# Optimization experiments

Measured on AMD Instinct MI355X. Metric: run time of the kernel, lower is better.

Reference implementation:

```python
import jax, jax.numpy as jnp
import numpy as np

BITS = 4
GROUP_SIZE = 128
INF, OUTF, TOKENS = 4096, 11008, 256


def setup_inputs() -> dict:
    key = jax.random.key(0)
    k1, k2, k3, k4, k5 = jax.random.split(key, 5)
    n_groups = INF // GROUP_SIZE  # 32
    x = jax.random.normal(k1, (TOKENS, INF), dtype=jnp.float32)
    qweight = jax.random.randint(k2, (INF // 32 * BITS, OUTF), 0, 2**31 - 1, dtype=jnp.int32)
    qzeros = jax.random.randint(k3, (n_groups, OUTF // 32 * BITS), 0, 2**31 - 1, dtype=jnp.int32)
    scales = jax.random.uniform(k4, (n_groups, OUTF), dtype=jnp.float32, minval=1e-3, maxval=2e-2)
    bias = jax.random.normal(k5, (OUTF,), dtype=jnp.float32)
    return {"x": x, "qweight": qweight, "qzeros": qzeros, "scales": scales, "bias": bias}


def _dequantize(qweight, qzeros, scales):
    """Unpack int4 nibbles and build the fp32 weight [infeatures, outfeatures]."""
    shifts = jnp.arange(0, 32, BITS, dtype=jnp.int32)  # [8]
    mask = (1 << BITS) - 1
    out_f = qweight.shape[1]
    # qweight row packs 8 consecutive in-features -> [K, O] int in [0, 15]
    w = ((qweight[:, None, :] >> shifts[None, :, None]) & mask).reshape(-1, out_f)
    # qzeros col packs 8 consecutive out-features; stored as (zero - 1)
    n_groups = qzeros.shape[0]
    z = (((qzeros[:, :, None] >> shifts[None, None, :]) & mask) + 1).reshape(n_groups, out_f)
    g_idx = jnp.arange(w.shape[0], dtype=jnp.int32) // GROUP_SIZE  # [K]
    return (w - z[g_idx]).astype(jnp.float32) * scales[g_idx]


def reference(x, qweight, qzeros, scales, bias):
    W = _dequantize(qweight, qzeros, scales)  # [infeatures, outfeatures]
    return x @ W + bias  # [tokens, outfeatures]
```

## Files before the change

### kernel.cpp

```cpp
#include <hip/hip_runtime.h>
#include <stdint.h>

#define TOKENS  256
#define INF     4096
#define OUTF    11008
#define NGROUPS 32
#define NPHASE  16
#define NTH     256

typedef __attribute__((ext_vector_type(2))) _Float16 f16x2;
typedef __attribute__((ext_vector_type(8))) _Float16 f16x8;
typedef __attribute__((ext_vector_type(2))) __fp16   pkh2;
typedef __attribute__((ext_vector_type(4))) float    f32x4;

union U32H2 { uint32_t u; f16x2 h; };
union H8    { f16x2 h2[4]; f16x8 h8; };
union PK    { pkh2 p; f16x2 h; };

__device__ __forceinline__ void gl2lds16(const void* g, void* l) {
    __builtin_amdgcn_global_load_lds(
        (const __attribute__((address_space(1))) uint32_t*)g,
        (__attribute__((address_space(3))) uint32_t*)l, 16, 0, 0);
}

__device__ __forceinline__ int Fswz(int m4) {
    return (m4 & 0xF) | (((m4 ^ (m4 >> 1)) & 1) << 4);
}

__global__ __launch_bounds__(NTH)
void cvt_x(const float* __restrict__ x, _Float16* __restrict__ x16) {
    const int t   = blockIdx.x * NTH + threadIdx.x;
    const int row = t >> 9;
    const int c   = t & 511;
    const float* p = x + (size_t)row * INF + c * 8;
    f32x4 v0 = *(const f32x4*)p;
    f32x4 v1 = *(const f32x4*)(p + 4);
    H8 o; PK k0, k1, k2, k3;
    k0.p = __builtin_amdgcn_cvt_pkrtz(v0[0], v1[0]);
    k1.p = __builtin_amdgcn_cvt_pkrtz(v0[1], v1[1]);
    k2.p = __builtin_amdgcn_cvt_pkrtz(v0[2], v1[2]);
    k3.p = __builtin_amdgcn_cvt_pkrtz(v0[3], v1[3]);
    o.h2[0] = k0.h; o.h2[1] = k1.h; o.h2[2] = k2.h; o.h2[3] = k3.h;
    *(f16x8*)(x16 + (size_t)row * INF + c * 8) = o.h8;
}

__global__ __launch_bounds__(NTH, 2)
void qlin_main(const _Float16* __restrict__ x16,
               const uint32_t* __restrict__ qweight,
               const uint32_t* __restrict__ qzeros,
               const float* __restrict__ scales,
               const float* __restrict__ bias,
               float* __restrict__ out)
{
    __shared__ alignas(16) _Float16 As[2][64 * 256];

    const int tid = threadIdx.x;
    const int bx  = blockIdx.x >> 2;
    const int by  = blockIdx.x & 3;

    const int lane = tid & 63;
    const int quad = lane >> 4;
    const int l16  = lane & 15;
    const int wv   = tid >> 6;

    const int rowoff = (tid >> 5) & 7;
    const int sclin  = tid & 31;
    const int row0   = by * 64;
    const uint32_t aoffE = (uint32_t)((row0 + rowoff)     * (INF * 2) + (sclin ^ Fswz(rowoff))     * 16);
    const uint32_t aoffO = (uint32_t)((row0 + 8 + rowoff) * (INF * 2) + (sclin ^ Fswz(8 + rowoff)) * 16);
    const char* x16b = (const char*)x16;
    _Float16* ldsW = &As[0][0];
    const int ldsSlotBase = wv * 512;

    const int col0 = bx * 128 + wv * 32 + l16;
    const int col1 = col0 + 16;
    const int bOff0 = quad * OUTF + col0;
    const int bOff1 = quad * OUTF + col1;
    const int zsh = (col0 & 7) * 4;

    const int fsw = Fswz(l16);

    f32x4 acc[4][2];
#pragma unroll
    for (int mi = 0; mi < 4; ++mi)
#pragma unroll
        for (int nf = 0; nf < 2; ++nf)
            acc[mi][nf] = f32x4{0.f, 0.f, 0.f, 0.f};

    uint32_t Breg[2][16];
    float    sS[2][4];
    uint32_t qZ[2][4];

#pragma unroll
    for (int ii = 0; ii < 4; ++ii) {
        gl2lds16(x16b + aoffE + ii * 131072, ldsW + (2 * ii)     * 2048 + ldsSlotBase);
        gl2lds16(x16b + aoffO + ii * 131072, ldsW + (2 * ii + 1) * 2048 + ldsSlotBase);
    }
#pragma unroll
    for (int s = 0; s < 8; ++s) {
        const uint32_t* qp = qweight + (size_t)(s * 4) * OUTF;
        Breg[0][2 * s + 0] = qp[bOff0];
        Breg[0][2 * s + 1] = qp[bOff1];
    }
    sS[0][0] = scales[0 * OUTF + col0]; sS[0][1] = scales[0 * OUTF + col1];
    sS[0][2] = scales[1 * OUTF + col0]; sS[0][3] = scales[1 * OUTF + col1];
    qZ[0][0] = qzeros[0 * (OUTF / 8) + (col0 >> 3)]; qZ[0][1] = qzeros[0 * (OUTF / 8) + (col1 >> 3)];
    qZ[0][2] = qzeros[1 * (OUTF / 8) + (col0 >> 3)]; qZ[0][3] = qzeros[1 * (OUTF / 8) + (col1 >> 3)];
    __syncthreads();

#pragma unroll
    for (int p = 0; p < NPHASE; ++p) {
        const int par = p & 1;
        const int np  = par ^ 1;

        if (p < NPHASE - 1) {
            const int pn = p + 1;
            const uint32_t pb = (uint32_t)(pn * 512);
            _Float16* ldsN = ldsW + np * 16384;
#pragma unroll
            for (int ii = 0; ii < 4; ++ii) {
                gl2lds16(x16b + aoffE + ii * 131072 + pb, ldsN + (2 * ii)     * 2048 + ldsSlotBase);
                gl2lds16(x16b + aoffO + ii * 131072 + pb, ldsN + (2 * ii + 1) * 2048 + ldsSlotBase);
            }
            const uint32_t* qpb = qweight + (size_t)(pn * 32) * OUTF;
#pragma unroll
            for (int s = 0; s < 8; ++s) {
                const uint32_t* qp = qpb + (size_t)(s * 4) * OUTF;
                Breg[np][2 * s + 0] = qp[bOff0];
                Breg[np][2 * s + 1] = qp[bOff1];
            }
            const int g0 = 2 * pn, g1 = 2 * pn + 1;
            sS[np][0] = scales[g0 * OUTF + col0]; sS[np][1] = scales[g0 * OUTF + col1];
            sS[np][2] = scales[g1 * OUTF + col0]; sS[np][3] = scales[g1 * OUTF + col1];
            qZ[np][0] = qzeros[g0 * (OUTF / 8) + (col0 >> 3)]; qZ[np][1] = qzeros[g0 * (OUTF / 8) + (col1 >> 3)];
            qZ[np][2] = qzeros[g1 * (OUTF / 8) + (col0 >> 3)]; qZ[np][3] = qzeros[g1 * (OUTF / 8) + (col1 >> 3)];
        }

        f16x2 hs2[2][2], hz2[2][2];
#pragma unroll
        for (int gh = 0; gh < 2; ++gh)
#pragma unroll
            for (int nf = 0; nf < 2; ++nf) {
                const float s = sS[par][gh * 2 + nf];
                const int   z = (int)((qZ[par][gh * 2 + nf] >> zsh) & 15u) + 1025;
                const _Float16 hs = (_Float16)s;
                const _Float16 hz = (_Float16)(-(float)z);
                hs2[gh][nf] = f16x2{hs, hs};
                hz2[gh][nf] = f16x2{hz, hz};
            }

        const _Float16* buf = ldsW + par * 16384;
#pragma unroll
        for (int s = 0; s < 8; ++s) {
            const int gh = s >> 2;
            f16x8 af[4];
#pragma unroll
            for (int mi = 0; mi < 4; ++mi) {
                const int m  = mi * 16 + l16;
                const int sc = (s * 4 + quad) ^ fsw;
                af[mi] = *(const f16x8*)(buf + m * 256 + sc * 8);
            }
#pragma unroll
            for (int nf = 0; nf < 2; ++nf) {
                const uint32_t q = Breg[par][2 * s + nf];
                H8 b;
#pragma unroll
                for (int j = 0; j < 4; ++j) {
                    U32H2 u;
                    u.u = ((q >> (4 * j)) & 0x000F000Fu) | 0x64006400u;
                    b.h2[j] = (u.h + hz2[gh][nf]) * hs2[gh][nf];
                }
#pragma unroll
                for (int mi = 0; mi < 4; ++mi)
                    acc[mi][nf] = __builtin_amdgcn_mfma_f32_16x16x32_f16(
                        af[mi], b.h8, acc[mi][nf], 0, 0, 0);
            }
        }

        __syncthreads();
    }

#pragma unroll
    for (int nf = 0; nf < 2; ++nf) {
        const int col = (nf == 0) ? col0 : col1;
        const float bv = bias[col];
#pragma unroll
        for (int mi = 0; mi < 4; ++mi) {
            const int r0 = by * 64 + mi * 16 + quad * 4;
#pragma unroll
            for (int rg = 0; rg < 4; ++rg)
                out[(size_t)(r0 + rg) * OUTF + col] = acc[mi][nf][rg] + bv;
        }
    }
}

__global__ __launch_bounds__(NTH, 2)
void qlin_fb(const float* __restrict__ x,
             const uint32_t* __restrict__ qweight,
             const uint32_t* __restrict__ qzeros,
             const float* __restrict__ scales,
             const float* __restrict__ bias,
             float* __restrict__ out)
{
    __shared__ alignas(16) _Float16 Asb[64][40];
    __shared__ alignas(16) _Float16 Bsb[128][40];
    const int tid = threadIdx.x;
    const int bx = blockIdx.x, by = blockIdx.y;
    const int am = tid >> 2, ar = tid & 3;
    const float* xrow = x + (size_t)(by * 64 + am) * INF + ar * 8;
    const int bc = tid & 127, br = tid >> 7;
    const int bn = bx * 128 + bc;
    const int bswz = (bc >> 3) & 3;
    const int lane = tid & 63, quad = lane >> 4, l16 = lane & 15;
    const int wv = tid >> 6, wm = wv >> 1, wn = wv & 1;
    f32x4 acc[2][4];
#pragma unroll
    for (int i = 0; i < 2; ++i)
#pragma unroll
        for (int j = 0; j < 4; ++j) acc[i][j] = f32x4{0.f, 0.f, 0.f, 0.f};
    f32x4 pa0 = *(const f32x4*)(xrow + 0);
    f32x4 pa1 = *(const f32x4*)(xrow + 4);
    uint32_t pq0 = qweight[(size_t)br * OUTF + bn];
    uint32_t pq1 = qweight[(size_t)(br + 2) * OUTF + bn];
    for (int g = 0; g < NGROUPS; ++g) {
        const float s = scales[g * OUTF + bn];
        const uint32_t qzv = qzeros[g * (OUTF / 8) + (bn >> 3)];
        const int z = (int)((qzv >> (4 * (bn & 7))) & 15u) + 1;
        const _Float16 hs = (_Float16)s;
        const _Float16 hz = (_Float16)(-(float)(1024 + z));
        const f16x2 hs2 = {hs, hs}, hz2 = {hz, hz};
#pragma unroll
        for (int t4 = 0; t4 < 4; ++t4) {
            const int it = (g << 2) + t4;
            { H8 ah; PK p0, p1, p2, p3;
              p0.p = __builtin_amdgcn_cvt_pkrtz(pa0[0], pa1[0]);
              p1.p = __builtin_amdgcn_cvt_pkrtz(pa0[1], pa1[1]);
              p2.p = __builtin_amdgcn_cvt_pkrtz(pa0[2], pa1[2]);
              p3.p = __builtin_amdgcn_cvt_pkrtz(pa0[3], pa1[3]);
              ah.h2[0] = p0.h; ah.h2[1] = p1.h; ah.h2[2] = p2.h; ah.h2[3] = p3.h;
              *(f16x8*)&Asb[am][ar * 8] = ah.h8; }
            { const uint32_t qq[2] = {pq0, pq1};
#pragma unroll
              for (int rr = 0; rr < 2; ++rr) {
                  const int r = br + rr * 2; H8 bh;
#pragma unroll
                  for (int jp = 0; jp < 4; ++jp) {
                      U32H2 u; u.u = ((qq[rr] >> (4 * jp)) & 0x000F000Fu) | 0x64006400u;
                      bh.h2[jp] = (u.h + hz2) * hs2;
                  }
                  *(f16x8*)&Bsb[bc][(r ^ bswz) * 8] = bh.h8;
              } }
            __syncthreads();
            const int itn = (it < 127) ? it + 1 : 127;
            pa0 = *(const f32x4*)(xrow + itn * 32);
            pa1 = *(const f32x4*)(xrow + itn * 32 + 4);
            pq0 = qweight[(size_t)(itn * 4 + br) * OUTF + bn];
            pq1 = qweight[(size_t)(itn * 4 + br + 2) * OUTF + bn];
            f16x8 af[2], bf[4];
#pragma unroll
            for (int mi = 0; mi < 2; ++mi)
                af[mi] = *(const f16x8*)&Asb[wm * 32 + mi * 16 + l16][quad * 8];
#pragma unroll
            for (int ni = 0; ni < 4; ++ni) {
                const int c = wn * 64 + ni * 16 + l16;
                bf[ni] = *(const f16x8*)&Bsb[c][(quad ^ ((c >> 3) & 3)) * 8];
            }
#pragma unroll
            for (int mi = 0; mi < 2; ++mi)
#pragma unroll
                for (int ni = 0; ni < 4; ++ni)
                    acc[mi][ni] = __builtin_amdgcn_mfma_f32_16x16x32_f16(
                        af[mi], bf[ni], acc[mi][ni], 0, 0, 0);
            __syncthreads();
        }
    }
#pragma unroll
    for (int ni = 0; ni < 4; ++ni) {
        const int col = bx * 128 + wn * 64 + ni * 16 + l16;
        const float bv = bias[col];
#pragma unroll
        for (int mi = 0; mi < 2; ++mi) {
            const int row0 = by * 64 + wm * 32 + mi * 16 + quad * 4;
#pragma unroll
            for (int rg = 0; rg < 4; ++rg)
                out[(size_t)(row0 + rg) * OUTF + col] = acc[mi][ni][rg] + bv;
        }
    }
}

extern "C" void kernel_launch(void* const* d_in, const int* in_sizes, int n_in,
                              void* d_out, int out_size, void* d_ws, size_t ws_size,
                              hipStream_t stream) {
    const float*    xx = (const float*)d_in[0];
    const uint32_t* qw = (const uint32_t*)d_in[1];
    const uint32_t* qz = (const uint32_t*)d_in[2];
    const float*    sc = (const float*)d_in[3];
    const float*    bs = (const float*)d_in[4];
    float* out = (float*)d_out;

    const size_t x16_bytes = (size_t)TOKENS * INF * sizeof(_Float16);
    if (ws_size >= x16_bytes) {
        _Float16* x16 = (_Float16*)d_ws;
        cvt_x<<<(TOKENS * INF / 8) / NTH, NTH, 0, stream>>>(xx, x16);
        qlin_main<<<(OUTF / 128) * (TOKENS / 64), NTH, 0, stream>>>(x16, qw, qz, sc, bs, out);
    } else {
        dim3 grid(OUTF / 128, TOKENS / 64);
        qlin_fb<<<grid, NTH, 0, stream>>>(xx, qw, qz, sc, bs, out);
    }
}
```

Before: 122.0 us.

## Split K across blocks with atomic accumulation and larger 128x128 tiles

Restructures the quantized GEMM into a split-K scheme. K is split 8 ways, each block computes a 128x128 output tile, and partial sums are combined with float atomicAdd into an output pre-filled with bias by a new init kernel. The aim is more blocks (1376 instead of 344), higher occupancy, and less redundant weight dequantization per token row. The cost is atomic traffic on the 11 MB output, an extra launch, and scales and zeros are now reloaded every phase instead of prefetched.

```diff
diff --git a/kernel.cpp b/kernel.cpp
--- a/kernel.cpp
+++ b/kernel.cpp
@@ -5,8 +5,12 @@
 #define INF     4096
 #define OUTF    11008
 #define NGROUPS 32
-#define NPHASE  16
 #define NTH     256
+
+#define KSPLIT  8
+#define KBLK    (INF / KSPLIT)
+#define PHK     64
+#define NPH     (KBLK / PHK)
 
 typedef __attribute__((ext_vector_type(2))) _Float16 f16x2;
 typedef __attribute__((ext_vector_type(8))) _Float16 f16x8;
@@ -21,10 +25,6 @@
     __builtin_amdgcn_global_load_lds(
         (const __attribute__((address_space(1))) uint32_t*)g,
         (__attribute__((address_space(3))) uint32_t*)l, 16, 0, 0);
-}
-
-__device__ __forceinline__ int Fswz(int m4) {
-    return (m4 & 0xF) | (((m4 ^ (m4 >> 1)) & 1) << 4);
 }
 
 __global__ __launch_bounds__(NTH)
@@ -44,152 +44,151 @@
     *(f16x8*)(x16 + (size_t)row * INF + c * 8) = o.h8;
 }
 
-__global__ __launch_bounds__(NTH, 2)
+__global__ __launch_bounds__(NTH)
+void init_out(const float* __restrict__ bias, float* __restrict__ out) {
+    const int idx = blockIdx.x * NTH + threadIdx.x;
+    const int c4  = idx - (idx / (OUTF / 4)) * (OUTF / 4);
+    ((f32x4*)out)[idx] = ((const f32x4*)bias)[c4];
+}
+
+__global__ __launch_bounds__(NTH, 4)
 void qlin_main(const _Float16* __restrict__ x16,
                const uint32_t* __restrict__ qweight,
                const uint32_t* __restrict__ qzeros,
                const float* __restrict__ scales,
-               const float* __restrict__ bias,
                float* __restrict__ out)
 {
-    __shared__ alignas(16) _Float16 As[2][64 * 256];
+    __shared__ alignas(16) _Float16 As[2][128 * PHK];
 
     const int tid = threadIdx.x;
-    const int bx  = blockIdx.x >> 2;
-    const int by  = blockIdx.x & 3;
+    const int b   = blockIdx.x;
+    const int kh  = b & 7;
+    const int by  = (b >> 3) & 1;
+    const int bx  = b >> 4;
 
     const int lane = tid & 63;
     const int quad = lane >> 4;
     const int l16  = lane & 15;
     const int wv   = tid >> 6;
-
-    const int rowoff = (tid >> 5) & 7;
-    const int sclin  = tid & 31;
-    const int row0   = by * 64;
-    const uint32_t aoffE = (uint32_t)((row0 + rowoff)     * (INF * 2) + (sclin ^ Fswz(rowoff))     * 16);
-    const uint32_t aoffO = (uint32_t)((row0 + 8 + rowoff) * (INF * 2) + (sclin ^ Fswz(8 + rowoff)) * 16);
+    const int wr   = wv >> 1;
+    const int wc   = wv & 1;
+
+    const int arow  = (tid >> 3);
+    const int lchk  = (tid & 7) ^ (arow & 7);
     const char* x16b = (const char*)x16;
+    uint32_t aoff[4];
+#pragma unroll
+    for (int ii = 0; ii < 4; ++ii)
+        aoff[ii] = (uint32_t)((by * 128 + ii * 32 + arow) * (INF * 2)
+                              + kh * (KBLK * 2) + lchk * 16);
     _Float16* ldsW = &As[0][0];
-    const int ldsSlotBase = wv * 512;
-
-    const int col0 = bx * 128 + wv * 32 + l16;
-    const int col1 = col0 + 16;
-    const int bOff0 = quad * OUTF + col0;
-    const int bOff1 = quad * OUTF + col1;
-    const int zsh = (col0 & 7) * 4;
-
-    const int fsw = Fswz(l16);
-
-    f32x4 acc[4][2];
+    const int ldsBase = wv * 512;
+
+    int colN[4];
+#pragma unroll
+    for (int nf = 0; nf < 4; ++nf)
+        colN[nf] = bx * 128 + wc * 64 + nf * 16 + l16;
+    const int zsh = (colN[0] & 7) * 4;
+    const int qrow0 = kh * (KBLK / 8);
+
+    f32x4 acc[4][4];
 #pragma unroll
     for (int mi = 0; mi < 4; ++mi)
 #pragma unroll
-        for (int nf = 0; nf < 2; ++nf)
+        for (int nf = 0; nf < 4; ++nf)
             acc[mi][nf] = f32x4{0.f, 0.f, 0.f, 0.f};
 
-    uint32_t Breg[2][16];
-    float    sS[2][4];
-    uint32_t qZ[2][4];
-
-#pragma unroll
-    for (int ii = 0; ii < 4; ++ii) {
-        gl2lds16(x16b + aoffE + ii * 131072, ldsW + (2 * ii)     * 2048 + ldsSlotBase);
-        gl2lds16(x16b + aoffO + ii * 131072, ldsW + (2 * ii + 1) * 2048 + ldsSlotBase);
-    }
-#pragma unroll
-    for (int s = 0; s < 8; ++s) {
-        const uint32_t* qp = qweight + (size_t)(s * 4) * OUTF;
-        Breg[0][2 * s + 0] = qp[bOff0];
-        Breg[0][2 * s + 1] = qp[bOff1];
-    }
-    sS[0][0] = scales[0 * OUTF + col0]; sS[0][1] = scales[0 * OUTF + col1];
-    sS[0][2] = scales[1 * OUTF + col0]; sS[0][3] = scales[1 * OUTF + col1];
-    qZ[0][0] = qzeros[0 * (OUTF / 8) + (col0 >> 3)]; qZ[0][1] = qzeros[0 * (OUTF / 8) + (col1 >> 3)];
-    qZ[0][2] = qzeros[1 * (OUTF / 8) + (col0 >> 3)]; qZ[0][3] = qzeros[1 * (OUTF / 8) + (col1 >> 3)];
+    uint32_t Breg[2][8];
+
+#pragma unroll
+    for (int ii = 0; ii < 4; ++ii)
+        gl2lds16(x16b + aoff[ii], ldsW + ii * 2048 + ldsBase);
+#pragma unroll
+    for (int s = 0; s < 2; ++s) {
+        const uint32_t* qp = qweight + (size_t)(qrow0 + s * 4 + quad) * OUTF;
+#pragma unroll
+        for (int nf = 0; nf < 4; ++nf)
+            Breg[0][s * 4 + nf] = qp[colN[nf]];
+    }
     __syncthreads();
 
-#pragma unroll
-    for (int p = 0; p < NPHASE; ++p) {
-        const int par = p & 1;
-        const int np  = par ^ 1;
-
-        if (p < NPHASE - 1) {
-            const int pn = p + 1;
-            const uint32_t pb = (uint32_t)(pn * 512);
-            _Float16* ldsN = ldsW + np * 16384;
-#pragma unroll
-            for (int ii = 0; ii < 4; ++ii) {
-                gl2lds16(x16b + aoffE + ii * 131072 + pb, ldsN + (2 * ii)     * 2048 + ldsSlotBase);
-                gl2lds16(x16b + aoffO + ii * 131072 + pb, ldsN + (2 * ii + 1) * 2048 + ldsSlotBase);
-            }
-            const uint32_t* qpb = qweight + (size_t)(pn * 32) * OUTF;
-#pragma unroll
-            for (int s = 0; s < 8; ++s) {
-                const uint32_t* qp = qpb + (size_t)(s * 4) * OUTF;
-                Breg[np][2 * s + 0] = qp[bOff0];
-                Breg[np][2 * s + 1] = qp[bOff1];
-            }
-            const int g0 = 2 * pn, g1 = 2 * pn + 1;
-            sS[np][0] = scales[g0 * OUTF + col0]; sS[np][1] = scales[g0 * OUTF + col1];
-            sS[np][2] = scales[g1 * OUTF + col0]; sS[np][3] = scales[g1 * OUTF + col1];
-            qZ[np][0] = qzeros[g0 * (OUTF / 8) + (col0 >> 3)]; qZ[np][1] = qzeros[g0 * (OUTF / 8) + (col1 >> 3)];
-            qZ[np][2] = qzeros[g1 * (OUTF / 8) + (col0 >> 3)]; qZ[np][3] = qzeros[g1 * (OUTF / 8) + (col1 >> 3)];
-        }
-
-        f16x2 hs2[2][2], hz2[2][2];
-#pragma unroll
-        for (int gh = 0; gh < 2; ++gh)
-#pragma unroll
-            for (int nf = 0; nf < 2; ++nf) {
-                const float s = sS[par][gh * 2 + nf];
-                const int   z = (int)((qZ[par][gh * 2 + nf] >> zsh) & 15u) + 1025;
-                const _Float16 hs = (_Float16)s;
-                const _Float16 hz = (_Float16)(-(float)z);
-                hs2[gh][nf] = f16x2{hs, hs};
-                hz2[gh][nf] = f16x2{hz, hz};
-            }
-
-        const _Float16* buf = ldsW + par * 16384;
-#pragma unroll
-        for (int s = 0; s < 8; ++s) {
-            const int gh = s >> 2;
-            f16x8 af[4];
-#pragma unroll
-            for (int mi = 0; mi < 4; ++mi) {
-                const int m  = mi * 16 + l16;
-                const int sc = (s * 4 + quad) ^ fsw;
-                af[mi] = *(const f16x8*)(buf + m * 256 + sc * 8);
-            }
-#pragma unroll
-            for (int nf = 0; nf < 2; ++nf) {
-                const uint32_t q = Breg[par][2 * s + nf];
-                H8 b;
-#pragma unroll
-                for (int j = 0; j < 4; ++j) {
-                    U32H2 u;
-                    u.u = ((q >> (4 * j)) & 0x000F000Fu) | 0x64006400u;
-                    b.h2[j] = (u.h + hz2[gh][nf]) * hs2[gh][nf];
-                }
-#pragma unroll
-                for (int mi = 0; mi < 4; ++mi)
-                    acc[mi][nf] = __builtin_amdgcn_mfma_f32_16x16x32_f16(
-                        af[mi], b.h8, acc[mi][nf], 0, 0, 0);
-            }
-        }
-
-        __syncthreads();
-    }
-
-#pragma unroll
-    for (int nf = 0; nf < 2; ++nf) {
-        const int col = (nf == 0) ? col0 : col1;
-        const float bv = bias[col];
+#define PHASE_BODY(PAR, P, DO_PREFETCH)                                         \
+    {                                                                           \
+        const int p_ = (P);                                                     \
+        if (DO_PREFETCH) {                                                      \
+            const int pn = p_ + 1;                                              \
+            _Float16* ldsN = ldsW + (1 - (PAR)) * 8192;                         \
+            _Pragma("unroll")                                                   \
+            for (int ii = 0; ii < 4; ++ii)                                      \
+                gl2lds16(x16b + aoff[ii] + pn * (PHK * 2),                      \
+                         ldsN + ii * 2048 + ldsBase);                           \
+            _Pragma("unroll")                                                   \
+            for (int s = 0; s < 2; ++s) {                                       \
+                const uint32_t* qp = qweight +                                  \
+                    (size_t)(qrow0 + pn * 8 + s * 4 + quad) * OUTF;             \
+                _Pragma("unroll")                                               \
+                for (int nf = 0; nf < 4; ++nf)                                  \
+                    Breg[1 - (PAR)][s * 4 + nf] = qp[colN[nf]];                 \
+            }                                                                   \
+        }                                                                       \
+                       \
+        const int g_ = kh * (KBLK / 128) + (p_ >> 1);                           \
+        f16x2 hs2[4], hz2[4];                                                   \
+        _Pragma("unroll")                                                       \
+        for (int nf = 0; nf < 4; ++nf) {                                        \
+            const float s = scales[g_ * OUTF + colN[nf]];                       \
+            const int   z = (int)((qzeros[g_ * (OUTF / 8) + (colN[nf] >> 3)]    \
+                                   >> zsh) & 15u) + 1025;                       \
+            const _Float16 hs = (_Float16)s;                                    \
+            const _Float16 hz = (_Float16)(-(float)z);                          \
+            hs2[nf] = f16x2{hs, hs};                                            \
+            hz2[nf] = f16x2{hz, hz};                                            \
+        }                                                                       \
+        const _Float16* buf = ldsW + (PAR) * 8192;                              \
+        _Pragma("unroll")                                                       \
+        for (int s = 0; s < 2; ++s) {                                           \
+            f16x8 af[4];                                                        \
+            _Pragma("unroll")                                                   \
+            for (int mi = 0; mi < 4; ++mi) {                                    \
+                const int m  = wr * 64 + mi * 16 + l16;                         \
+                const int sc = (s * 4 + quad) ^ (l16 & 7);                      \
+                af[mi] = *(const f16x8*)(buf + m * PHK + sc * 8);               \
+            }                                                                   \
+            _Pragma("unroll")                                                   \
+            for (int nf = 0; nf < 4; ++nf) {                                    \
+                const uint32_t q = Breg[PAR][s * 4 + nf];                       \
+                H8 bfr;                                                         \
+                _Pragma("unroll")                                               \
+                for (int j = 0; j < 4; ++j) {                                   \
+                    U32H2 u;                                                    \
+                    u.u = ((q >> (4 * j)) & 0x000F000Fu) | 0x64006400u;         \
+                    bfr.h2[j] = (u.h + hz2[nf]) * hs2[nf];                      \
+                }                                                               \
+                _Pragma("unroll")                                               \
+                for (int mi = 0; mi < 4; ++mi)                                  \
+                    acc[mi][nf] = __builtin_amdgcn_mfma_f32_16x16x32_f16(       \
+                        af[mi], bfr.h8, acc[mi][nf], 0, 0, 0);                  \
+            }                                                                   \
+        }                                                                       \
+        __syncthreads();                                                        \
+    }
+
+#pragma unroll 1
+    for (int pp = 0; pp < NPH / 2; ++pp) {
+        PHASE_BODY(0, 2 * pp, true)
+        PHASE_BODY(1, 2 * pp + 1, (pp < NPH / 2 - 1))
+    }
+#undef PHASE_BODY
+
+#pragma unroll
+    for (int nf = 0; nf < 4; ++nf) {
+        const int col = colN[nf];
 #pragma unroll
         for (int mi = 0; mi < 4; ++mi) {
-            const int r0 = by * 64 + mi * 16 + quad * 4;
+            const int r0 = by * 128 + wr * 64 + mi * 16 + quad * 4;
 #pragma unroll
             for (int rg = 0; rg < 4; ++rg)
-                out[(size_t)(r0 + rg) * OUTF + col] = acc[mi][nf][rg] + bv;
+                atomicAdd(&out[(size_t)(r0 + rg) * OUTF + col], acc[mi][nf][rg]);
         }
     }
 }
@@ -302,7 +301,8 @@
     if (ws_size >= x16_bytes) {
         _Float16* x16 = (_Float16*)d_ws;
         cvt_x<<<(TOKENS * INF / 8) / NTH, NTH, 0, stream>>>(xx, x16);
-        qlin_main<<<(OUTF / 128) * (TOKENS / 64), NTH, 0, stream>>>(x16, qw, qz, sc, bs, out);
+        init_out<<<(TOKENS * OUTF / 4) / NTH, NTH, 0, stream>>>(bs, out);
+        qlin_main<<<(OUTF / 128) * 2 * KSPLIT, NTH, 0, stream>>>(x16, qw, qz, sc, out);
     } else {
         dim3 grid(OUTF / 128, TOKENS / 64);
         qlin_fb<<<grid, NTH, 0, stream>>>(xx, qw, qz, sc, bs, out);
```

After: 235.4 us. 1.93x slower.

## Replace LDS-staged 256-thread GEMM with single-wave blocks loading A directly to registers

Applied to the files above, without the earlier changes.

Removes the shared-memory double buffer and block barriers. Each block is now one 64-lane wave covering 64 tokens by 32 output columns. Activations are loaded from global memory straight into registers with a software-pipelined register ring (A four steps ahead, packed weights eight steps ahead), and scales/zeros are prefetched two groups ahead. This drops the synchronisation and LDS traffic, but activation rows are no longer shared across waves, so L2 reads of x16 rise about fourfold and the grid grows to 1376 small blocks.

```diff
diff --git a/kernel.cpp b/kernel.cpp
--- a/kernel.cpp
+++ b/kernel.cpp
@@ -5,7 +5,6 @@
 #define INF     4096
 #define OUTF    11008
 #define NGROUPS 32
-#define NPHASE  16
 #define NTH     256
 
 typedef __attribute__((ext_vector_type(2))) _Float16 f16x2;
@@ -16,16 +15,6 @@
 union U32H2 { uint32_t u; f16x2 h; };
 union H8    { f16x2 h2[4]; f16x8 h8; };
 union PK    { pkh2 p; f16x2 h; };
-
-__device__ __forceinline__ void gl2lds16(const void* g, void* l) {
-    __builtin_amdgcn_global_load_lds(
-        (const __attribute__((address_space(1))) uint32_t*)g,
-        (__attribute__((address_space(3))) uint32_t*)l, 16, 0, 0);
-}
-
-__device__ __forceinline__ int Fswz(int m4) {
-    return (m4 & 0xF) | (((m4 ^ (m4 >> 1)) & 1) << 4);
-}
 
 __global__ __launch_bounds__(NTH)
 void cvt_x(const float* __restrict__ x, _Float16* __restrict__ x16) {
@@ -44,41 +33,26 @@
     *(f16x8*)(x16 + (size_t)row * INF + c * 8) = o.h8;
 }
 
-__global__ __launch_bounds__(NTH, 2)
-void qlin_main(const _Float16* __restrict__ x16,
+__global__ __launch_bounds__(64, 2)
+void qlin_wave(const _Float16* __restrict__ x16,
                const uint32_t* __restrict__ qweight,
                const uint32_t* __restrict__ qzeros,
                const float* __restrict__ scales,
                const float* __restrict__ bias,
                float* __restrict__ out)
 {
-    __shared__ alignas(16) _Float16 As[2][64 * 256];
-
-    const int tid = threadIdx.x;
-    const int bx  = blockIdx.x >> 2;
-    const int by  = blockIdx.x & 3;
-
-    const int lane = tid & 63;
+    const int lane = threadIdx.x;
+    const int bx   = blockIdx.x;
+    const int by   = blockIdx.y;
+
     const int quad = lane >> 4;
     const int l16  = lane & 15;
-    const int wv   = tid >> 6;
-
-    const int rowoff = (tid >> 5) & 7;
-    const int sclin  = tid & 31;
-    const int row0   = by * 64;
-    const uint32_t aoffE = (uint32_t)((row0 + rowoff)     * (INF * 2) + (sclin ^ Fswz(rowoff))     * 16);
-    const uint32_t aoffO = (uint32_t)((row0 + 8 + rowoff) * (INF * 2) + (sclin ^ Fswz(8 + rowoff)) * 16);
-    const char* x16b = (const char*)x16;
-    _Float16* ldsW = &As[0][0];
-    const int ldsSlotBase = wv * 512;
-
-    const int col0 = bx * 128 + wv * 32 + l16;
+
+    const _Float16* abase = x16 + (size_t)(by * 64 + l16) * INF + quad * 8;
+
+    const int col0 = bx * 32 + l16;
     const int col1 = col0 + 16;
-    const int bOff0 = quad * OUTF + col0;
-    const int bOff1 = quad * OUTF + col1;
-    const int zsh = (col0 & 7) * 4;
-
-    const int fsw = Fswz(l16);
+    const int zsh  = (col0 & 7) * 4;
 
     f32x4 acc[4][2];
 #pragma unroll
@@ -87,97 +61,86 @@
         for (int nf = 0; nf < 2; ++nf)
             acc[mi][nf] = f32x4{0.f, 0.f, 0.f, 0.f};
 
-    uint32_t Breg[2][16];
-    float    sS[2][4];
-    uint32_t qZ[2][4];
-
-#pragma unroll
-    for (int ii = 0; ii < 4; ++ii) {
-        gl2lds16(x16b + aoffE + ii * 131072, ldsW + (2 * ii)     * 2048 + ldsSlotBase);
-        gl2lds16(x16b + aoffO + ii * 131072, ldsW + (2 * ii + 1) * 2048 + ldsSlotBase);
-    }
+    f16x8    af[4][4];
+    uint32_t Breg[8][2];
+    float    sS[2][2];
+    uint32_t qZ[2][2];
+
+#pragma unroll
+    for (int s = 0; s < 4; ++s)
+#pragma unroll
+        for (int mi = 0; mi < 4; ++mi)
+            af[s][mi] = *(const f16x8*)(abase + (size_t)mi * (16 * INF) + s * 32);
 #pragma unroll
     for (int s = 0; s < 8; ++s) {
-        const uint32_t* qp = qweight + (size_t)(s * 4) * OUTF;
-        Breg[0][2 * s + 0] = qp[bOff0];
-        Breg[0][2 * s + 1] = qp[bOff1];
-    }
-    sS[0][0] = scales[0 * OUTF + col0]; sS[0][1] = scales[0 * OUTF + col1];
-    sS[0][2] = scales[1 * OUTF + col0]; sS[0][3] = scales[1 * OUTF + col1];
-    qZ[0][0] = qzeros[0 * (OUTF / 8) + (col0 >> 3)]; qZ[0][1] = qzeros[0 * (OUTF / 8) + (col1 >> 3)];
-    qZ[0][2] = qzeros[1 * (OUTF / 8) + (col0 >> 3)]; qZ[0][3] = qzeros[1 * (OUTF / 8) + (col1 >> 3)];
-    __syncthreads();
-
-#pragma unroll
-    for (int p = 0; p < NPHASE; ++p) {
-        const int par = p & 1;
-        const int np  = par ^ 1;
-
-        if (p < NPHASE - 1) {
-            const int pn = p + 1;
-            const uint32_t pb = (uint32_t)(pn * 512);
-            _Float16* ldsN = ldsW + np * 16384;
-#pragma unroll
-            for (int ii = 0; ii < 4; ++ii) {
-                gl2lds16(x16b + aoffE + ii * 131072 + pb, ldsN + (2 * ii)     * 2048 + ldsSlotBase);
-                gl2lds16(x16b + aoffO + ii * 131072 + pb, ldsN + (2 * ii + 1) * 2048 + ldsSlotBase);
-            }
-            const uint32_t* qpb = qweight + (size_t)(pn * 32) * OUTF;
-#pragma unroll
-            for (int s = 0; s < 8; ++s) {
-                const uint32_t* qp = qpb + (size_t)(s * 4) * OUTF;
-                Breg[np][2 * s + 0] = qp[bOff0];
-                Breg[np][2 * s + 1] = qp[bOff1];
-            }
-            const int g0 = 2 * pn, g1 = 2 * pn + 1;
-            sS[np][0] = scales[g0 * OUTF + col0]; sS[np][1] = scales[g0 * OUTF + col1];
-            sS[np][2] = scales[g1 * OUTF + col0]; sS[np][3] = scales[g1 * OUTF + col1];
-            qZ[np][0] = qzeros[g0 * (OUTF / 8) + (col0 >> 3)]; qZ[np][1] = qzeros[g0 * (OUTF / 8) + (col1 >> 3)];
-            qZ[np][2] = qzeros[g1 * (OUTF / 8) + (col0 >> 3)]; qZ[np][3] = qzeros[g1 * (OUTF / 8) + (col1 >> 3)];
-        }
-
-        f16x2 hs2[2][2], hz2[2][2];
-#pragma unroll
-        for (int gh = 0; gh < 2; ++gh)
+        const uint32_t* qp = qweight + (size_t)(s * 4 + quad) * OUTF;
+        Breg[s][0] = qp[col0];
+        Breg[s][1] = qp[col1];
+    }
+#pragma unroll
+    for (int g = 0; g < 2; ++g) {
+        sS[g][0] = scales[g * OUTF + col0];
+        sS[g][1] = scales[g * OUTF + col1];
+        qZ[g][0] = qzeros[g * (OUTF / 8) + (col0 >> 3)];
+        qZ[g][1] = qzeros[g * (OUTF / 8) + (col1 >> 3)];
+    }
+
+#pragma unroll 1
+    for (int g = 0; g < NGROUPS; ++g) {
+        f16x2 hs2[2], hz2[2];
+#pragma unroll
+        for (int nf = 0; nf < 2; ++nf) {
+            const float s = sS[g & 1][nf];
+            const int   z = (int)((qZ[g & 1][nf] >> zsh) & 15u) + 1025;
+            const _Float16 hs = (_Float16)s;
+            const _Float16 hz = (_Float16)(-(float)z);
+            hs2[nf] = f16x2{hs, hs};
+            hz2[nf] = f16x2{hz, hz};
+        }
+        {
+            const int gn = (g + 2 < NGROUPS) ? g + 2 : NGROUPS - 1;
+            sS[g & 1][0] = scales[gn * OUTF + col0];
+            sS[g & 1][1] = scales[gn * OUTF + col1];
+            qZ[g & 1][0] = qzeros[gn * (OUTF / 8) + (col0 >> 3)];
+            qZ[g & 1][1] = qzeros[gn * (OUTF / 8) + (col1 >> 3)];
+        }
+
+#pragma unroll
+        for (int j = 0; j < 4; ++j) {
+            const int s = 4 * g + j;
+
+            H8 bfr[2];
 #pragma unroll
             for (int nf = 0; nf < 2; ++nf) {
-                const float s = sS[par][gh * 2 + nf];
-                const int   z = (int)((qZ[par][gh * 2 + nf] >> zsh) & 15u) + 1025;
-                const _Float16 hs = (_Float16)s;
-                const _Float16 hz = (_Float16)(-(float)z);
-                hs2[gh][nf] = f16x2{hs, hs};
-                hz2[gh][nf] = f16x2{hz, hz};
-            }
-
-        const _Float16* buf = ldsW + par * 16384;
-#pragma unroll
-        for (int s = 0; s < 8; ++s) {
-            const int gh = s >> 2;
-            f16x8 af[4];
+                const uint32_t q = Breg[s & 7][nf];
+#pragma unroll
+                for (int jp = 0; jp < 4; ++jp) {
+                    U32H2 u;
+                    u.u = ((q >> (4 * jp)) & 0x000F000Fu) | 0x64006400u;
+                    bfr[nf].h2[jp] = (u.h + hz2[nf]) * hs2[nf];
+                }
+            }
+
 #pragma unroll
             for (int mi = 0; mi < 4; ++mi) {
-                const int m  = mi * 16 + l16;
-                const int sc = (s * 4 + quad) ^ fsw;
-                af[mi] = *(const f16x8*)(buf + m * 256 + sc * 8);
-            }
-#pragma unroll
-            for (int nf = 0; nf < 2; ++nf) {
-                const uint32_t q = Breg[par][2 * s + nf];
-                H8 b;
-#pragma unroll
-                for (int j = 0; j < 4; ++j) {
-                    U32H2 u;
-                    u.u = ((q >> (4 * j)) & 0x000F000Fu) | 0x64006400u;
-                    b.h2[j] = (u.h + hz2[gh][nf]) * hs2[gh][nf];
-                }
-#pragma unroll
-                for (int mi = 0; mi < 4; ++mi)
+#pragma unroll
+                for (int nf = 0; nf < 2; ++nf)
                     acc[mi][nf] = __builtin_amdgcn_mfma_f32_16x16x32_f16(
-                        af[mi], b.h8, acc[mi][nf], 0, 0, 0);
-            }
-        }
-
-        __syncthreads();
+                        af[s & 3][mi], bfr[nf].h8, acc[mi][nf], 0, 0, 0);
+            }
+
+            const int sA = (s + 4 < 128) ? s + 4 : 127;
+            const int sB = (s + 8 < 128) ? s + 8 : 127;
+#pragma unroll
+            for (int mi = 0; mi < 4; ++mi)
+                af[s & 3][mi] = *(const f16x8*)(abase + (size_t)mi * (16 * INF)
+                                                + sA * 32);
+            {
+                const uint32_t* qp = qweight + (size_t)(sB * 4 + quad) * OUTF;
+                Breg[s & 7][0] = qp[col0];
+                Breg[s & 7][1] = qp[col1];
+            }
+        }
     }
 
 #pragma unroll
@@ -302,7 +265,8 @@
     if (ws_size >= x16_bytes) {
         _Float16* x16 = (_Float16*)d_ws;
         cvt_x<<<(TOKENS * INF / 8) / NTH, NTH, 0, stream>>>(xx, x16);
-        qlin_main<<<(OUTF / 128) * (TOKENS / 64), NTH, 0, stream>>>(x16, qw, qz, sc, bs, out);
+        dim3 grid(OUTF / 32, TOKENS / 64);
+        qlin_wave<<<grid, 64, 0, stream>>>(x16, qw, qz, sc, bs, out);
     } else {
         dim3 grid(OUTF / 128, TOKENS / 64);
         qlin_fb<<<grid, NTH, 0, stream>>>(xx, qw, qz, sc, bs, out);
```

After: 181.2 us. +48.5%, slower.
